# Performance work log

Measured on AMD Instinct MI355X. Metric: run time of the kernel, lower is better.

Reference implementation:

```python
import jax, jax.numpy as jnp
import numpy as np

N, IN_FEAT, D1, D2, NUM_CLASSES = 8192, 2048, 512, 128, 10


def setup_inputs() -> dict:
    key = jax.random.key(0)
    ks = jax.random.split(key, 12)

    def xavier(k, shape):
        fan_in, fan_out = shape[1], shape[0]
        lim = np.sqrt(6.0 / (fan_in + fan_out))
        return jax.random.uniform(k, shape, jnp.float32, -lim, lim)

    return {
        "x": jax.random.normal(ks[0], (N, 1, IN_FEAT), jnp.float32),
        "W1": xavier(ks[1], (D1, IN_FEAT)), "b1": jnp.zeros((D1,), jnp.float32),
        "W2": xavier(ks[2], (D2, D1)), "b2": jnp.zeros((D2,), jnp.float32),
        # conv1d kernel_size=1 weights, squeezed to (out, in)
        "Wq": jax.random.normal(ks[3], (D2, D2), jnp.float32) * 0.05,
        "bq": jnp.zeros((D2,), jnp.float32),
        "Wk": jax.random.normal(ks[4], (D2, D2), jnp.float32) * 0.05,
        "bk": jnp.zeros((D2,), jnp.float32),
        "gamma": jnp.ones((1,), jnp.float32),
        "W3": xavier(ks[5], (NUM_CLASSES, D2)), "b3": jnp.zeros((NUM_CLASSES,), jnp.float32),
    }


def reference(x, W1, b1, W2, b2, Wq, bq, Wk, bk, gamma, W3, b3):
    # MLP stack over patches: (N, 1, in) -> (N, 1, 128)
    h = jax.nn.relu(jnp.einsum("nbi,oi->nbo", x, W1) + b1)
    h = jax.nn.relu(jnp.einsum("nbi,oi->nbo", h, W2) + b2)
    # permute(1, 2, 0): (1, C, N)
    xp = jnp.transpose(h, (1, 2, 0))
    # 1x1 conv projections (pointwise linear over channels)
    q = jnp.einsum("oc,bcn->bno", Wq, xp) + bq            # (1, N, C)
    k = jnp.einsum("oc,bcn->bcn", Wk, xp) + bk[None, :, None]  # (1, C, N)
    energy = jnp.einsum("bnc,bcm->bnm", q, k)             # (1, N, N)
    attention = jax.nn.softmax(energy, axis=-1)
    # out = bmm(x, attention^T): (1, C, N)
    out = jnp.einsum("bcm,bnm->bcn", xp, attention)
    out = gamma * out + xp
    x2 = out.mean(axis=-1)                                 # (1, C)
    logits = x2 @ W3.T + b3                                # (1, num_classes)
    return (logits, attention)
```

## Files before the change

### kernel.cpp

```cpp
#include <hip/hip_runtime.h>
#include <hip/hip_bf16.h>

typedef __attribute__((ext_vector_type(8))) __bf16 bf16x8;
typedef __attribute__((ext_vector_type(4))) __bf16 bf16x4;
typedef __attribute__((ext_vector_type(4))) float f32x4;

#define N_TOK 8192
#define IN_FEAT 2048
#define D1 512
#define D2 128
#define QBLK 128
#define KCHUNK 1024
#define KTILE 128
#define NKC (N_TOK / KCHUNK)
#define NQB (N_TOK / QBLK)

__device__ __forceinline__ void gload_lds16(const __bf16* g, __bf16* l) {
    __builtin_amdgcn_global_load_lds(
        (const __attribute__((address_space(1))) void*)g,
        (__attribute__((address_space(3))) void*)l,
        16, 0, 0);
}

__device__ __forceinline__ void stage_tile(const __bf16* __restrict__ g,
                                           __bf16* lds, int w, int lane) {
#pragma unroll
    for (int i = 0; i < 8; ++i) {
        int row   = i * 16 + w * 4 + (lane >> 4);
        int chunk = (lane & 15) ^ (row & 7);
        gload_lds16(g + (size_t)row * 128 + chunk * 8, lds + i * 2048 + w * 512);
    }
}

__device__ __forceinline__ bf16x8 rd_frag(const __bf16* lds, int row, int chunk) {
    return *(const bf16x8*)(lds + row * 128 + ((chunk ^ (row & 7)) * 8));
}

__global__ __launch_bounds__(256)
void prep(const float* __restrict__ W1, __bf16* __restrict__ w1b,
          const float* __restrict__ W2, __bf16* __restrict__ w2b,
          const float* __restrict__ Wq, __bf16* __restrict__ wqb,
          const float* __restrict__ Wk, float* __restrict__ wksum,
          float* __restrict__ colw, float* __restrict__ xw, float* __restrict__ xh) {
    int b = blockIdx.x, t = threadIdx.x;
    const float* src = nullptr; __bf16* dst = nullptr; int i = 0;
    if (b < 1024)      { src = W1; dst = w1b; i = b * 256 + t; }
    else if (b < 1088) { src = W2; dst = w2b; i = (b - 1024) * 256 + t; }
    else if (b < 1104) { src = Wq; dst = wqb; i = (b - 1088) * 256 + t; }
    else if (b < 1136) { colw[(b - 1104) * 256 + t] = 0.0f; return; }
    else {
        if (t < D2) {
            float s = 0.0f;
            for (int o = 0; o < D2; ++o) s += Wk[o * D2 + t];
            wksum[t] = s;
            xw[t] = 0.0f; xh[t] = 0.0f;
        }
        return;
    }
    float4 v = ((const float4*)src)[i];
    bf16x4 o;
    o[0] = (__bf16)v.x; o[1] = (__bf16)v.y; o[2] = (__bf16)v.z; o[3] = (__bf16)v.w;
    ((bf16x4*)dst)[i] = o;
}

__global__ __launch_bounds__(256)
void gemm1_k(const float* __restrict__ x, const __bf16* __restrict__ w1b,
             const float* __restrict__ b1, __bf16* __restrict__ h1b) {
    __shared__ __bf16 lA[128 * 32];
    __shared__ __bf16 lB[64 * 32];

    const int t    = threadIdx.x;
    const int lane = t & 63;
    const int w    = t >> 6;
    const int wr   = w >> 1;
    const int wc   = w & 1;
    const int m0   = blockIdx.y * 128;
    const int n0   = blockIdx.x * 64;

    const int rS = w * 16 + (lane >> 2);
    const int cS = (lane & 3) * 8;
    const int fr = lane & 15;
    const int hi = lane >> 4;
    const int ko = hi * 8;
    const int rj = hi * 4;

    f32x4 acc[4][2] = {};

    for (int k0 = 0; k0 < IN_FEAT; k0 += 32) {
        float4 regs[4];
#pragma unroll
        for (int i = 0; i < 4; ++i) {
            int r = i * 32 + (t >> 3);
            regs[i] = *(const float4*)&x[(size_t)(m0 + r) * IN_FEAT + k0 + (t & 7) * 4];
        }
        __syncthreads();
#pragma unroll
        for (int i = 0; i < 4; ++i) {
            int r = i * 32 + (t >> 3);
            bf16x4 o;
            o[0] = (__bf16)regs[i].x; o[1] = (__bf16)regs[i].y;
            o[2] = (__bf16)regs[i].z; o[3] = (__bf16)regs[i].w;
            *(bf16x4*)&lA[r * 32 + (t & 7) * 4] = o;
        }
        gload_lds16(w1b + (size_t)(n0 + rS) * IN_FEAT + k0 + cS, lB + w * 512);
        __syncthreads();

        bf16x8 af[4], bf[2];
#pragma unroll
        for (int m = 0; m < 4; ++m)
            af[m] = *(const bf16x8*)&lA[(wr * 64 + m * 16 + fr) * 32 + ko];
#pragma unroll
        for (int n = 0; n < 2; ++n)
            bf[n] = *(const bf16x8*)&lB[(wc * 32 + n * 16 + fr) * 32 + ko];
#pragma unroll
        for (int m = 0; m < 4; ++m)
#pragma unroll
            for (int n = 0; n < 2; ++n)
                acc[m][n] = __builtin_amdgcn_mfma_f32_16x16x32_bf16(af[m], bf[n], acc[m][n], 0, 0, 0);
    }

#pragma unroll
    for (int n = 0; n < 2; ++n) {
        int col = n0 + wc * 32 + n * 16 + fr;
        float bv = b1[col];
#pragma unroll
        for (int m = 0; m < 4; ++m) {
            int row = m0 + wr * 64 + m * 16 + rj;
#pragma unroll
            for (int j = 0; j < 4; ++j)
                h1b[(size_t)(row + j) * D1 + col] = (__bf16)fmaxf(acc[m][n][j] + bv, 0.0f);
        }
    }
}

__global__ __launch_bounds__(256)
void mlp2_k(const __bf16* __restrict__ h1b, const __bf16* __restrict__ w2b,
            const float* __restrict__ b2, const __bf16* __restrict__ wqb,
            const float* __restrict__ bq, const float* __restrict__ wksum,
            const float* __restrict__ bk, __bf16* __restrict__ h2b,
            __bf16* __restrict__ kb, __bf16* __restrict__ qb) {
    __shared__ __bf16 lA[32 * 32];
    __shared__ __bf16 lB[128 * 32];
    __shared__ __bf16 lH[32 * 128];

    const int t    = threadIdx.x;
    const int lane = t & 63;
    const int w    = t >> 6;
    const int fr   = lane & 15;
    const int hi   = lane >> 4;
    const int ko   = hi * 8;
    const int m0   = blockIdx.x * 32;

    f32x4 acc[2][2] = {};

    for (int k0 = 0; k0 < D1; k0 += 32) {
        __syncthreads();
        if (w < 2)
            gload_lds16(h1b + (size_t)(m0 + w * 16 + (lane >> 2)) * D1 + k0 + (lane & 3) * 8,
                        lA + w * 512);
#pragma unroll
        for (int i = 0; i < 2; ++i) {
            int row = w * 32 + i * 16 + (lane >> 2);
            gload_lds16(w2b + (size_t)row * D1 + k0 + (lane & 3) * 8,
                        lB + w * 1024 + i * 512);
        }
        __syncthreads();

        bf16x8 af[2], bf[2];
#pragma unroll
        for (int m = 0; m < 2; ++m)
            af[m] = *(const bf16x8*)&lA[(m * 16 + fr) * 32 + ko];
#pragma unroll
        for (int n = 0; n < 2; ++n)
            bf[n] = *(const bf16x8*)&lB[(w * 32 + n * 16 + fr) * 32 + ko];
#pragma unroll
        for (int m = 0; m < 2; ++m)
#pragma unroll
            for (int n = 0; n < 2; ++n)
                acc[m][n] = __builtin_amdgcn_mfma_f32_16x16x32_bf16(af[m], bf[n], acc[m][n], 0, 0, 0);
    }

#pragma unroll
    for (int n = 0; n < 2; ++n) {
        int col = w * 32 + n * 16 + fr;
        float bv = b2[col], wv = wksum[col], bkv = bk[col];
#pragma unroll
        for (int m = 0; m < 2; ++m) {
#pragma unroll
            for (int j = 0; j < 4; ++j) {
                int row = m * 16 + hi * 4 + j;
                float v = fmaxf(acc[m][n][j] + bv, 0.0f);
                h2b[(size_t)(m0 + row) * D2 + col] = (__bf16)v;
                kb [(size_t)(m0 + row) * D2 + col] = (__bf16)(wv * v + bkv);
                lH[row * 128 + (((col >> 3) ^ (row & 7)) * 8) + (col & 7)] = (__bf16)v;
            }
        }
    }
    __syncthreads();

    f32x4 acc2[2][2] = {};
#pragma unroll
    for (int kk = 0; kk < 4; ++kk) {
        bf16x8 af2[2], bf2[2];
#pragma unroll
        for (int m = 0; m < 2; ++m) {
            int row = m * 16 + fr;
            af2[m] = *(const bf16x8*)&lH[row * 128 + (((kk * 4 + hi) ^ (row & 7)) * 8)];
        }
#pragma unroll
        for (int n = 0; n < 2; ++n)
            bf2[n] = *(const bf16x8*)&wqb[(size_t)(w * 32 + n * 16 + fr) * D2 + kk * 32 + ko];
#pragma unroll
        for (int m = 0; m < 2; ++m)
#pragma unroll
            for (int n = 0; n < 2; ++n)
                acc2[m][n] = __builtin_amdgcn_mfma_f32_16x16x32_bf16(af2[m], bf2[n], acc2[m][n], 0, 0, 0);
    }
#pragma unroll
    for (int n = 0; n < 2; ++n) {
        int col = w * 32 + n * 16 + fr;
        float bv = bq[col];
#pragma unroll
        for (int m = 0; m < 2; ++m)
#pragma unroll
            for (int j = 0; j < 4; ++j) {
                int row = m0 + m * 16 + hi * 4 + j;
                qb[(size_t)row * D2 + col] = (__bf16)(acc2[m][n][j] + bv);
            }
    }
}

template<int PASS>
__global__ __launch_bounds__(256, 2)
void fa_kernel(const __bf16* __restrict__ qbuf, const __bf16* __restrict__ kbuf,
               float* __restrict__ pm, float* __restrict__ pl,
               const float* __restrict__ rowM, const float* __restrict__ rowInv,
               float* __restrict__ attn, float* __restrict__ colw)
{
    __shared__ __bf16 Kl[2][KTILE * 128];

    const int t    = threadIdx.x;
    const int lane = t & 63;
    const int w    = t >> 6;
    const int wr   = w >> 1;
    const int wc   = w & 1;
    const int fr   = lane & 15;
    const int hi   = lane >> 4;
    const int ck   = blockIdx.x;
    const int q0   = blockIdx.y * QBLK;
    const int kr0  = ck * KCHUNK;

    stage_tile(qbuf + (size_t)q0 * D2, Kl[0], w, lane);
    __syncthreads();
    bf16x8 af[4][4];
#pragma unroll
    for (int m = 0; m < 4; ++m)
#pragma unroll
        for (int kk = 0; kk < 4; ++kk)
            af[m][kk] = rd_frag(Kl[0], wr * 64 + m * 16 + fr, kk * 4 + hi);
    __syncthreads();

    float mloc[4][4], lloc[4][4], Mr[4][4], Ir[4][4];
#pragma unroll
    for (int m = 0; m < 4; ++m)
#pragma unroll
        for (int j = 0; j < 4; ++j) {
            if constexpr (PASS == 1) { mloc[m][j] = -1e30f; lloc[m][j] = 0.0f; }
            else {
                int r = q0 + wr * 64 + m * 16 + hi * 4 + j;
                Mr[m][j] = rowM[r]; Ir[m][j] = rowInv[r];
            }
        }

    stage_tile(kbuf + (size_t)kr0 * D2, Kl[0], w, lane);
    __syncthreads();

    for (int kt = 0; kt < KCHUNK / KTILE; ++kt) {
        const __bf16* cur = Kl[kt & 1];
        if (kt + 1 < KCHUNK / KTILE)
            stage_tile(kbuf + (size_t)(kr0 + (kt + 1) * KTILE) * D2, Kl[(kt + 1) & 1], w, lane);

        f32x4 acc[4][4] = {};
#pragma unroll
        for (int kk = 0; kk < 4; ++kk) {
            bf16x8 bfr[4];
#pragma unroll
            for (int n = 0; n < 4; ++n)
                bfr[n] = rd_frag(cur, wc * 64 + n * 16 + fr, kk * 4 + hi);
#pragma unroll
            for (int m = 0; m < 4; ++m)
#pragma unroll
                for (int n = 0; n < 4; ++n)
                    acc[m][n] = __builtin_amdgcn_mfma_f32_16x16x32_bf16(af[m][kk], bfr[n], acc[m][n], 0, 0, 0);
        }

        if constexpr (PASS == 1) {
#pragma unroll
            for (int m = 0; m < 4; ++m)
#pragma unroll
                for (int j = 0; j < 4; ++j) {
                    float a0 = acc[m][0][j], a1 = acc[m][1][j], a2 = acc[m][2][j], a3 = acc[m][3][j];
                    float t4 = fmaxf(fmaxf(a0, a1), fmaxf(a2, a3));
                    float mo = mloc[m][j];
                    float mn = fmaxf(mo, t4);
                    float s  = __expf(a0 - mn) + __expf(a1 - mn) + __expf(a2 - mn) + __expf(a3 - mn);
                    lloc[m][j] = lloc[m][j] * __expf(mo - mn) + s;
                    mloc[m][j] = mn;
                }
        } else {
            float csum[4] = {0.0f, 0.0f, 0.0f, 0.0f};
            const int colbase = kr0 + kt * KTILE + wc * 64;
#pragma unroll
            for (int m = 0; m < 4; ++m) {
#pragma unroll
                for (int n = 0; n < 4; ++n) {
                    int col = colbase + n * 16 + fr;
#pragma unroll
                    for (int j = 0; j < 4; ++j) {
                        int row = q0 + wr * 64 + m * 16 + hi * 4 + j;
                        float p = __expf(acc[m][n][j] - Mr[m][j]) * Ir[m][j];
                        attn[(size_t)row * N_TOK + col] = p;
                        csum[n] += p;
                    }
                }
            }
#pragma unroll
            for (int n = 0; n < 4; ++n) {
                csum[n] += __shfl_xor(csum[n], 16);
                csum[n] += __shfl_xor(csum[n], 32);
            }
            if (lane < 16) {
#pragma unroll
                for (int n = 0; n < 4; ++n)
                    atomicAdd(&colw[colbase + n * 16 + lane], csum[n]);
            }
        }
        __syncthreads();
    }

    if constexpr (PASS == 1) {
        const size_t slot = (size_t)(ck * 2 + wc) * N_TOK;
#pragma unroll
        for (int m = 0; m < 4; ++m)
#pragma unroll
            for (int j = 0; j < 4; ++j) {
                float M = mloc[m][j];
#pragma unroll
                for (int off = 1; off <= 8; off <<= 1) M = fmaxf(M, __shfl_xor(M, off));
                float l = lloc[m][j] * __expf(mloc[m][j] - M);
#pragma unroll
                for (int off = 1; off <= 8; off <<= 1) l += __shfl_xor(l, off);
                if ((lane & 15) == 0) {
                    int r = q0 + wr * 64 + m * 16 + hi * 4 + j;
                    pm[slot + r] = M;
                    pl[slot + r] = l;
                }
            }
    }
}

__global__ __launch_bounds__(256)
void combine_ml(const float* __restrict__ pm, const float* __restrict__ pl,
                float* __restrict__ rowM, float* __restrict__ rowInv) {
    int r = blockIdx.x * 256 + threadIdx.x;
    float M = -1e30f;
#pragma unroll
    for (int c = 0; c < 2 * NKC; ++c) M = fmaxf(M, pm[(size_t)c * N_TOK + r]);
    float L = 0.0f;
#pragma unroll
    for (int c = 0; c < 2 * NKC; ++c)
        L += pl[(size_t)c * N_TOK + r] * __expf(pm[(size_t)c * N_TOK + r] - M);
    rowM[r] = M;
    rowInv[r] = 1.0f / L;
}

__global__ __launch_bounds__(256)
void reduce_x2(const __bf16* __restrict__ h2b, const float* __restrict__ colw,
               float* __restrict__ xw, float* __restrict__ xh) {
    int b = blockIdx.x, t = threadIdx.x;
    int c = t & 127, half = t >> 7;
    float aw = 0.0f, ah = 0.0f;
    for (int m = b * 128 + half; m < (b + 1) * 128; m += 2) {
        float h  = (float)h2b[(size_t)m * D2 + c];
        float wv = colw[m];
        aw += wv * h;
        ah += h;
    }
    atomicAdd(&xw[c], aw);
    atomicAdd(&xh[c], ah);
}

__global__ void logits_k(const float* __restrict__ xw, const float* __restrict__ xh,
                         const float* __restrict__ gamma, const float* __restrict__ W3,
                         const float* __restrict__ b3, float* __restrict__ out) {
    __shared__ float x2[D2];
    int t = threadIdx.x;
    float g = gamma[0];
    if (t < D2) x2[t] = (g * xw[t] + xh[t]) * (1.0f / (float)N_TOK);
    __syncthreads();
    if (t < 10) {
        float s = b3[t];
        for (int c = 0; c < D2; ++c) s += x2[c] * W3[t * D2 + c];
        out[t] = s;
    }
}

extern "C" void kernel_launch(void* const* d_in, const int* in_sizes, int n_in,
                              void* d_out, int out_size, void* d_ws, size_t ws_size,
                              hipStream_t stream) {
    const float* x     = (const float*)d_in[0];
    const float* W1    = (const float*)d_in[1];
    const float* b1    = (const float*)d_in[2];
    const float* W2    = (const float*)d_in[3];
    const float* b2    = (const float*)d_in[4];
    const float* Wq    = (const float*)d_in[5];
    const float* bq    = (const float*)d_in[6];
    const float* Wk    = (const float*)d_in[7];
    const float* bk    = (const float*)d_in[8];
    const float* gamma = (const float*)d_in[9];
    const float* W3    = (const float*)d_in[10];
    const float* b3    = (const float*)d_in[11];

    float* out  = (float*)d_out;
    float* attn = out + 10;

    char* p = (char*)d_ws;
    __bf16* w1b = (__bf16*)p; p += (size_t)D1 * IN_FEAT * 2;
    __bf16* w2b = (__bf16*)p; p += (size_t)D2 * D1 * 2;
    __bf16* wqb = (__bf16*)p; p += (size_t)D2 * D2 * 2;
    __bf16* h1b = (__bf16*)p; p += (size_t)N_TOK * D1 * 2;
    __bf16* h2b = (__bf16*)p; p += (size_t)N_TOK * D2 * 2;
    __bf16* qb  = (__bf16*)p; p += (size_t)N_TOK * D2 * 2;
    __bf16* kb  = (__bf16*)p; p += (size_t)N_TOK * D2 * 2;
    float* pm     = (float*)p; p += (size_t)2 * NKC * N_TOK * 4;
    float* pl     = (float*)p; p += (size_t)2 * NKC * N_TOK * 4;
    float* rowM   = (float*)p; p += N_TOK * 4;
    float* rowInv = (float*)p; p += N_TOK * 4;
    float* colw   = (float*)p; p += N_TOK * 4;
    float* wksum  = (float*)p; p += D2 * 4;
    float* xw     = (float*)p; p += D2 * 4;
    float* xh     = (float*)p; p += D2 * 4;

    prep<<<1137, 256, 0, stream>>>(W1, w1b, W2, w2b, Wq, wqb, Wk, wksum, colw, xw, xh);

    gemm1_k<<<dim3(D1 / 64, N_TOK / 128), 256, 0, stream>>>(x, w1b, b1, h1b);
    mlp2_k<<<N_TOK / 32, 256, 0, stream>>>(h1b, w2b, b2, wqb, bq, wksum, bk, h2b, kb, qb);

    fa_kernel<1><<<dim3(NKC, NQB), 256, 0, stream>>>(
        qb, kb, pm, pl, nullptr, nullptr, nullptr, nullptr);
    combine_ml<<<N_TOK / 256, 256, 0, stream>>>(pm, pl, rowM, rowInv);
    fa_kernel<2><<<dim3(NKC, NQB), 256, 0, stream>>>(
        qb, kb, nullptr, nullptr, rowM, rowInv, attn, colw);

    reduce_x2<<<64, 256, 0, stream>>>(h2b, colw, xw, xh);
    logits_k<<<1, 128, 0, stream>>>(xw, xh, gamma, W3, b3, out);
}
```

Before: 301.7 us.

## Prefetch x into registers in gemm1, remap blocks, fuse softmax-stat combine into pass 2

In gemm1, the next k-slice of x is loaded into registers after the LDS barrier so the global load overlaps the MFMA work of the current slice. The 2D grid is flattened, with consecutive blocks sharing the same W1 column tile and walking the row tiles. The separate combine_ml launch is removed: each pass-2 attention block recomputes the row max and normalizer for its 128 rows from the partials and keeps them in LDS. This saves a launch and the rowM/rowInv round trip, at the cost of redundant per-block combine work (8 column-chunk blocks per row block) and more live registers in gemm1.

```diff
diff --git a/kernel.cpp b/kernel.cpp
--- a/kernel.cpp
+++ b/kernel.cpp
@@ -74,8 +74,9 @@
     const int w    = t >> 6;
     const int wr   = w >> 1;
     const int wc   = w & 1;
-    const int m0   = blockIdx.y * 128;
-    const int n0   = blockIdx.x * 64;
+    const int b    = blockIdx.x;
+    const int m0   = (b & 63) * 128;
+    const int n0   = (b >> 6) * 64;
 
     const int rS = w * 16 + (lane >> 2);
     const int cS = (lane & 3) * 8;
@@ -84,26 +85,33 @@
     const int ko = hi * 8;
     const int rj = hi * 4;
 
+    const int ar = t >> 3;
+    const int ac = (t & 7) * 4;
+
     f32x4 acc[4][2] = {};
 
+    float4 regs[4];
+#pragma unroll
+    for (int i = 0; i < 4; ++i)
+        regs[i] = *(const float4*)&x[(size_t)(m0 + i * 32 + ar) * IN_FEAT + ac];
+
     for (int k0 = 0; k0 < IN_FEAT; k0 += 32) {
-        float4 regs[4];
+        __syncthreads();
 #pragma unroll
         for (int i = 0; i < 4; ++i) {
-            int r = i * 32 + (t >> 3);
-            regs[i] = *(const float4*)&x[(size_t)(m0 + r) * IN_FEAT + k0 + (t & 7) * 4];
-        }
-        __syncthreads();
-#pragma unroll
-        for (int i = 0; i < 4; ++i) {
-            int r = i * 32 + (t >> 3);
             bf16x4 o;
             o[0] = (__bf16)regs[i].x; o[1] = (__bf16)regs[i].y;
             o[2] = (__bf16)regs[i].z; o[3] = (__bf16)regs[i].w;
-            *(bf16x4*)&lA[r * 32 + (t & 7) * 4] = o;
+            *(bf16x4*)&lA[(i * 32 + ar) * 32 + ac] = o;
         }
         gload_lds16(w1b + (size_t)(n0 + rS) * IN_FEAT + k0 + cS, lB + w * 512);
         __syncthreads();
+
+        if (k0 + 32 < IN_FEAT) {
+#pragma unroll
+            for (int i = 0; i < 4; ++i)
+                regs[i] = *(const float4*)&x[(size_t)(m0 + i * 32 + ar) * IN_FEAT + k0 + 32 + ac];
+        }
 
         bf16x8 af[4], bf[2];
 #pragma unroll
@@ -234,10 +242,10 @@
 __global__ __launch_bounds__(256, 2)
 void fa_kernel(const __bf16* __restrict__ qbuf, const __bf16* __restrict__ kbuf,
                float* __restrict__ pm, float* __restrict__ pl,
-               const float* __restrict__ rowM, const float* __restrict__ rowInv,
                float* __restrict__ attn, float* __restrict__ colw)
 {
     __shared__ __bf16 Kl[2][KTILE * 128];
+    __shared__ float rowM_l[QBLK], rowInv_l[QBLK];
 
     const int t    = threadIdx.x;
     const int lane = t & 63;
@@ -258,6 +266,21 @@
 #pragma unroll
         for (int kk = 0; kk < 4; ++kk)
             af[m][kk] = rd_frag(Kl[0], wr * 64 + m * 16 + fr, kk * 4 + hi);
+
+    if constexpr (PASS == 2) {
+        if (t < QBLK) {
+            int r = q0 + t;
+            float M = -1e30f;
+#pragma unroll
+            for (int c = 0; c < 2 * NKC; ++c) M = fmaxf(M, pm[(size_t)c * N_TOK + r]);
+            float L = 0.0f;
+#pragma unroll
+            for (int c = 0; c < 2 * NKC; ++c)
+                L += pl[(size_t)c * N_TOK + r] * __expf(pm[(size_t)c * N_TOK + r] - M);
+            rowM_l[t] = M;
+            rowInv_l[t] = 1.0f / L;
+        }
+    }
     __syncthreads();
 
     float mloc[4][4], lloc[4][4], Mr[4][4], Ir[4][4];
@@ -267,8 +290,8 @@
         for (int j = 0; j < 4; ++j) {
             if constexpr (PASS == 1) { mloc[m][j] = -1e30f; lloc[m][j] = 0.0f; }
             else {
-                int r = q0 + wr * 64 + m * 16 + hi * 4 + j;
-                Mr[m][j] = rowM[r]; Ir[m][j] = rowInv[r];
+                int rl = wr * 64 + m * 16 + hi * 4 + j;
+                Mr[m][j] = rowM_l[rl]; Ir[m][j] = rowInv_l[rl];
             }
         }
 
@@ -357,21 +380,6 @@
                 }
             }
     }
-}
-
-__global__ __launch_bounds__(256)
-void combine_ml(const float* __restrict__ pm, const float* __restrict__ pl,
-                float* __restrict__ rowM, float* __restrict__ rowInv) {
-    int r = blockIdx.x * 256 + threadIdx.x;
-    float M = -1e30f;
-#pragma unroll
-    for (int c = 0; c < 2 * NKC; ++c) M = fmaxf(M, pm[(size_t)c * N_TOK + r]);
-    float L = 0.0f;
-#pragma unroll
-    for (int c = 0; c < 2 * NKC; ++c)
-        L += pl[(size_t)c * N_TOK + r] * __expf(pm[(size_t)c * N_TOK + r] - M);
-    rowM[r] = M;
-    rowInv[r] = 1.0f / L;
 }
 
 __global__ __launch_bounds__(256)
@@ -434,8 +442,6 @@
     __bf16* kb  = (__bf16*)p; p += (size_t)N_TOK * D2 * 2;
     float* pm     = (float*)p; p += (size_t)2 * NKC * N_TOK * 4;
     float* pl     = (float*)p; p += (size_t)2 * NKC * N_TOK * 4;
-    float* rowM   = (float*)p; p += N_TOK * 4;
-    float* rowInv = (float*)p; p += N_TOK * 4;
     float* colw   = (float*)p; p += N_TOK * 4;
     float* wksum  = (float*)p; p += D2 * 4;
     float* xw     = (float*)p; p += D2 * 4;
@@ -443,14 +449,11 @@
 
     prep<<<1137, 256, 0, stream>>>(W1, w1b, W2, w2b, Wq, wqb, Wk, wksum, colw, xw, xh);
 
-    gemm1_k<<<dim3(D1 / 64, N_TOK / 128), 256, 0, stream>>>(x, w1b, b1, h1b);
+    gemm1_k<<<512, 256, 0, stream>>>(x, w1b, b1, h1b);
     mlp2_k<<<N_TOK / 32, 256, 0, stream>>>(h1b, w2b, b2, wqb, bq, wksum, bk, h2b, kb, qb);
 
-    fa_kernel<1><<<dim3(NKC, NQB), 256, 0, stream>>>(
-        qb, kb, pm, pl, nullptr, nullptr, nullptr, nullptr);
-    combine_ml<<<N_TOK / 256, 256, 0, stream>>>(pm, pl, rowM, rowInv);
-    fa_kernel<2><<<dim3(NKC, NQB), 256, 0, stream>>>(
-        qb, kb, nullptr, nullptr, rowM, rowInv, attn, colw);
+    fa_kernel<1><<<dim3(NKC, NQB), 256, 0, stream>>>(qb, kb, pm, pl, nullptr, nullptr);
+    fa_kernel<2><<<dim3(NKC, NQB), 256, 0, stream>>>(qb, kb, pm, pl, attn, colw);
 
     reduce_x2<<<64, 256, 0, stream>>>(h2b, colw, xw, xh);
     logits_k<<<1, 128, 0, stream>>>(xw, xh, gamma, W3, b3, out);
```

Result: faster. 292.5 us (-3.1%).
